# Kernel optimization log

Hardware: AMD Instinct MI355X
Metric: run time of the kernel (lower is better)

Reference implementation:

```python
import jax, jax.numpy as jnp
import numpy as np

EPS = 1e-5

def _bn(x, gamma, beta):
    # BatchNorm with track_running_stats=False: batch stats over all dims but last
    axes = tuple(range(x.ndim - 1))
    mu = jnp.mean(x, axis=axes)
    var = jnp.var(x, axis=axes)  # biased, as torch uses for normalization
    return (x - mu) * jax.lax.rsqrt(var + EPS) * gamma + beta

def setup_inputs() -> dict:
    B, N, D = 8, 200, 128
    key = jax.random.key(0)
    ks = jax.random.split(key, 14)
    s = 1.0 / np.sqrt(D)
    def w(k):
        return jax.random.uniform(k, (D, D), jnp.float32, -s, s)
    def b(k):
        return jax.random.uniform(k, (D,), jnp.float32, -s, s)
    return {
        'h': jax.random.normal(ks[0], (B, N, D), jnp.float32),
        'e': jax.random.normal(ks[1], (B, N, N, D), jnp.float32),
        'Uw': w(ks[2]), 'Ub': b(ks[3]),
        'Vw': w(ks[4]), 'Vb': b(ks[5]),
        'Aw': w(ks[6]), 'Ab': b(ks[7]),
        'Bw': w(ks[8]), 'Bb': b(ks[9]),
        'Cw': w(ks[10]), 'Cb': b(ks[11]),
        'gamma_h': jnp.ones((D,), jnp.float32), 'beta_h': jnp.zeros((D,), jnp.float32),
        'gamma_e': jnp.ones((D,), jnp.float32), 'beta_e': jnp.zeros((D,), jnp.float32),
    }

def reference(h, e, Uw, Ub, Vw, Vb, Aw, Ab, Bw, Bb, Cw, Cb,
              gamma_h, beta_h, gamma_e, beta_e):
    h_in, e_in = h, e
    Uh = h @ Uw.T + Ub                      # [B,N,D]
    Vh = h @ Vw.T + Vb                      # [B,N,D]
    Ah = h @ Aw.T + Ab
    Bh = h @ Bw.T + Bb
    Ce = e @ Cw.T + Cb                      # [B,N,N,D]
    # e_new[b,i,j,d] = Ah[b,j,d] + Bh[b,i,d] + Ce[b,i,j,d]
    e_new = Ah[:, None, :, :] + Bh[:, :, None, :] + Ce
    gates = jax.nn.sigmoid(e_new)           # [B,N,N,D]
    # sum aggregation over source nodes j with Vh broadcast over i
    agg = jnp.sum(gates * Vh[:, None, :, :], axis=2)  # [B,N,D]
    h_new = Uh + agg
    h_out = h_in + jax.nn.relu(_bn(h_new, gamma_h, beta_h))
    e_out = e_in + jax.nn.relu(_bn(e_new, gamma_e, beta_e))
    return (h_out, e_out)
```

## Files before the change

### kernel.cpp

```cpp
#include <hip/hip_runtime.h>
#include <hip/hip_bf16.h>


#define B_ 8
#define N_ 200
#define D_ 128
#define BN_ (B_*N_)
#define HN_ (BN_*D_)
#define EN_ (BN_*N_*D_)

typedef __attribute__((ext_vector_type(8))) short short8v;
typedef __attribute__((ext_vector_type(4))) short short4v;
typedef __attribute__((ext_vector_type(4))) float float4v;
typedef __attribute__((ext_vector_type(4))) unsigned int uint4v;

__device__ __forceinline__ unsigned short f2b(float f) {
  unsigned u = __float_as_uint(f);
  u += 0x7FFFu + ((u >> 16) & 1u);
  return (unsigned short)(u >> 16);
}

__global__ __launch_bounds__(256) void prelin_kernel(
    const float* __restrict__ h,
    const float* __restrict__ Uw, const float* __restrict__ Ub,
    const float* __restrict__ Vw, const float* __restrict__ Vb,
    const float* __restrict__ Aw, const float* __restrict__ Ab,
    const float* __restrict__ Bw, const float* __restrict__ Bb,
    const float* __restrict__ Cw,
    float* __restrict__ Uh, float* __restrict__ Vh,
    float* __restrict__ Ah, float* __restrict__ Bh,
    unsigned short* __restrict__ Cwbf) {
  const int tid = threadIdx.x;
  if (blockIdx.x >= 100) {
    int g = (blockIdx.x - 100) * 1024 + tid * 4;
    float4v v = *(const float4v*)(Cw + g);
    short4v s;
    s.x = (short)f2b(v.x); s.y = (short)f2b(v.y);
    s.z = (short)f2b(v.z); s.w = (short)f2b(v.w);
    *(short4v*)(Cwbf + g) = s;
    return;
  }
  const int r0 = blockIdx.x * 16;
  __shared__ float hs[16][128];
  for (int k = 0; k < 2; k++) {
    int g = k * 256 + tid;
    int row = g >> 5, col4 = g & 31;
    *(float4v*)&hs[row][col4 * 4] =
        *(const float4v*)(h + (size_t)(r0 + row) * D_ + col4 * 4);
  }
  __syncthreads();
  const int c0 = tid, c1 = tid + 256;
  const float* w0 = (c0 < 128) ? (Uw + c0 * 128) : (Vw + (c0 - 128) * 128);
  const float  b0 = (c0 < 128) ? Ub[c0] : Vb[c0 - 128];
  const float* w1 = (c1 < 384) ? (Aw + (c1 - 256) * 128) : (Bw + (c1 - 384) * 128);
  const float  b1 = (c1 < 384) ? Ab[c1 - 256] : Bb[c1 - 384];
  float acc0[16], acc1[16];
#pragma unroll
  for (int r = 0; r < 16; r++) { acc0[r] = 0.f; acc1[r] = 0.f; }
  for (int k = 0; k < 128; k += 4) {
    float4v w0v = *(const float4v*)(w0 + k);
    float4v w1v = *(const float4v*)(w1 + k);
#pragma unroll
    for (int r = 0; r < 16; r++) {
      float4v hv = *(const float4v*)&hs[r][k];
      acc0[r] = fmaf(hv.x, w0v.x, fmaf(hv.y, w0v.y, fmaf(hv.z, w0v.z, fmaf(hv.w, w0v.w, acc0[r]))));
      acc1[r] = fmaf(hv.x, w1v.x, fmaf(hv.y, w1v.y, fmaf(hv.z, w1v.z, fmaf(hv.w, w1v.w, acc1[r]))));
    }
  }
  float* dst0 = (c0 < 128) ? Uh : Vh; const int cc0 = c0 & 127;
  float* dst1 = (c1 < 384) ? Ah : Bh; const int cc1 = (c1 - 256) & 127;
#pragma unroll
  for (int r = 0; r < 16; r++) {
    dst0[(size_t)(r0 + r) * D_ + cc0] = acc0[r] + b0;
    dst1[(size_t)(r0 + r) * D_ + cc1] = acc1[r] + b1;
  }
}

template <int MODE>
__global__ __launch_bounds__(256, 2) void gemm_pass(
    const float* __restrict__ e, const unsigned short* __restrict__ Cwbf,
    const float* __restrict__ Cb, const float* __restrict__ Ah,
    const float* __restrict__ Bh, const float* __restrict__ Vh,
    float* __restrict__ agg, float* __restrict__ psum, float* __restrict__ psumsq,
    const float* __restrict__ scale_e, const float* __restrict__ shift_e,
    float* __restrict__ e_out) {
  const int tid = threadIdx.x;
  const int blk = blockIdx.x;
  const int b = blk / N_;
  const int lane = tid & 63, wz = tid >> 6;
  const int c = lane & 15, q = lane >> 4;

  __shared__ __align__(16) unsigned short Bs[128 * 136];
  __shared__ __align__(16) unsigned short As[64 * 136];
  __shared__ float base_s[128];
  __shared__ float ss_s[256];

  const uint4v* bsrc = (const uint4v*)Cwbf;
#pragma unroll
  for (int k2 = 0; k2 < 8; k2++) {
    int g = k2 * 256 + tid;
    int row = g >> 4, col = (g & 15) * 8;
    *(uint4v*)&Bs[row * 136 + col] = bsrc[g];
  }
  if (tid < 128) {
    base_s[tid] = Cb[tid] + Bh[(size_t)blk * D_ + tid];
    if (MODE == 1) { ss_s[tid] = scale_e[tid]; ss_s[128 + tid] = shift_e[tid]; }
  }

  float aggv[8], sumv[8], sqv[8];
  if (MODE == 0) {
#pragma unroll
    for (int t = 0; t < 8; t++) { aggv[t] = 0.f; sumv[t] = 0.f; sqv[t] = 0.f; }
  }

  const float* erow = e + (size_t)blk * N_ * D_;
  const float* AhB = Ah + (size_t)b * N_ * D_;
  const float* VhB = (MODE == 0) ? (Vh + (size_t)b * N_ * D_) : nullptr;

  for (int jt = 0; jt < 4; jt++) {
    const int j0 = jt * 64;
    __syncthreads();
#pragma unroll
    for (int k2 = 0; k2 < 8; k2++) {
      int g = k2 * 256 + tid;
      int row = g >> 5, col4 = g & 31;
      int j = j0 + row;
      float4v v;
      if (j < N_) v = *(const float4v*)(erow + (size_t)j * D_ + col4 * 4);
      else        v = (float4v){0.f, 0.f, 0.f, 0.f};
      short4v sv;
      sv.x = (short)f2b(v.x); sv.y = (short)f2b(v.y);
      sv.z = (short)f2b(v.z); sv.w = (short)f2b(v.w);
      *(short4v*)&As[row * 136 + col4 * 4] = sv;
    }
    __syncthreads();

    float4v acc[8];
#pragma unroll
    for (int t = 0; t < 8; t++) acc[t] = (float4v){0.f, 0.f, 0.f, 0.f};
    const unsigned short* arow = &As[(wz * 16 + c) * 136];
    const int ko = q * 8;
#pragma unroll
    for (int kk = 0; kk < 128; kk += 32) {
      short8v av = *(const short8v*)(arow + kk + ko);
#pragma unroll
      for (int t = 0; t < 8; t++) {
        short8v bv = *(const short8v*)&Bs[(t * 16 + c) * 136 + kk + ko];
        acc[t] = __builtin_amdgcn_mfma_f32_16x16x32_bf16(av, bv, acc[t], 0, 0, 0);
      }
    }

#pragma unroll
    for (int t = 0; t < 8; t++) {
      const int n = t * 16 + c;
      const float bse = base_s[n];
      float sc = 0.f, sh = 0.f;
      if (MODE == 1) { sc = ss_s[n]; sh = ss_s[128 + n]; }
#pragma unroll
      for (int r = 0; r < 4; r++) {
        const int j = j0 + wz * 16 + q * 4 + r;
        if (j < N_) {
          float x = acc[t][r] + bse + AhB[(size_t)j * D_ + n];
          if (MODE == 0) {
            float g = __builtin_amdgcn_rcpf(1.0f + __expf(-x));
            aggv[t] += g * VhB[(size_t)j * D_ + n];
            sumv[t] += x;
            sqv[t] += x * x;
          } else {
            float y = fmaxf(x * sc + sh, 0.f);
            size_t idx = (size_t)blk * N_ * D_ + (size_t)j * D_ + n;
            e_out[idx] = e[idx] + y;
          }
        }
      }
    }
  }

  if (MODE == 0) {
    __syncthreads();
    float* red = (float*)As;
#pragma unroll
    for (int t = 0; t < 8; t++) {
      float a = aggv[t], s = sumv[t], sq = sqv[t];
      a += __shfl_xor(a, 16); a += __shfl_xor(a, 32);
      s += __shfl_xor(s, 16); s += __shfl_xor(s, 32);
      sq += __shfl_xor(sq, 16); sq += __shfl_xor(sq, 32);
      if (q == 0) {
        red[(0 * 4 + wz) * 128 + t * 16 + c] = a;
        red[(1 * 4 + wz) * 128 + t * 16 + c] = s;
        red[(2 * 4 + wz) * 128 + t * 16 + c] = sq;
      }
    }
    __syncthreads();
    if (tid < 128) {
      float a = 0.f, s = 0.f, sq = 0.f;
#pragma unroll
      for (int w = 0; w < 4; w++) {
        a += red[(0 * 4 + w) * 128 + tid];
        s += red[(1 * 4 + w) * 128 + tid];
        sq += red[(2 * 4 + w) * 128 + tid];
      }
      agg[(size_t)blk * D_ + tid] = a;
      psum[(size_t)blk * D_ + tid] = s;
      psumsq[(size_t)blk * D_ + tid] = sq;
    }
  }
}

__global__ __launch_bounds__(256) void stats_kernel(
    const float* __restrict__ psum, const float* __restrict__ psumsq,
    const float* __restrict__ Uh, const float* __restrict__ agg,
    const float* __restrict__ gamma_h, const float* __restrict__ beta_h,
    const float* __restrict__ gamma_e, const float* __restrict__ beta_e,
    float* __restrict__ scale_e, float* __restrict__ shift_e,
    float* __restrict__ scale_h, float* __restrict__ shift_h) {
  const int n = blockIdx.x, t = threadIdx.x;
  float s = 0.f, sq = 0.f, hs = 0.f, hsq = 0.f;
  for (int k = t; k < BN_; k += 256) {
    s += psum[(size_t)k * D_ + n];
    sq += psumsq[(size_t)k * D_ + n];
    float hv = Uh[(size_t)k * D_ + n] + agg[(size_t)k * D_ + n];
    hs += hv; hsq += hv * hv;
  }
  __shared__ float r4[4][256];
  r4[0][t] = s; r4[1][t] = sq; r4[2][t] = hs; r4[3][t] = hsq;
  __syncthreads();
  for (int off = 128; off > 0; off >>= 1) {
    if (t < off) {
      r4[0][t] += r4[0][t + off]; r4[1][t] += r4[1][t + off];
      r4[2][t] += r4[2][t + off]; r4[3][t] += r4[3][t + off];
    }
    __syncthreads();
  }
  if (t == 0) {
    const float Me = (float)(B_ * N_ * N_);
    float mean = r4[0][0] / Me;
    float var = r4[1][0] / Me - mean * mean;
    float sce = gamma_e[n] * rsqrtf(var + 1e-5f);
    scale_e[n] = sce; shift_e[n] = beta_e[n] - mean * sce;
    const float Mh = (float)BN_;
    float mh = r4[2][0] / Mh;
    float vh = r4[3][0] / Mh - mh * mh;
    float sch = gamma_h[n] * rsqrtf(vh + 1e-5f);
    scale_h[n] = sch; shift_h[n] = beta_h[n] - mh * sch;
  }
}

__global__ __launch_bounds__(256) void hpath_kernel(
    const float* __restrict__ h, const float* __restrict__ Uh,
    const float* __restrict__ agg, const float* __restrict__ scale_h,
    const float* __restrict__ shift_h, float* __restrict__ h_out) {
  const int idx = blockIdx.x * 256 + threadIdx.x;
  float4v u = ((const float4v*)Uh)[idx];
  float4v a = ((const float4v*)agg)[idx];
  float4v hv = ((const float4v*)h)[idx];
  float4v sc = ((const float4v*)scale_h)[idx & 31];
  float4v sh = ((const float4v*)shift_h)[idx & 31];
  float4v o;
#pragma unroll
  for (int l = 0; l < 4; l++) {
    float y = fmaxf((u[l] + a[l]) * sc[l] + sh[l], 0.f);
    o[l] = hv[l] + y;
  }
  ((float4v*)h_out)[idx] = o;
}

extern "C" void kernel_launch(void* const* d_in, const int* in_sizes, int n_in,
                              void* d_out, int out_size, void* d_ws, size_t ws_size,
                              hipStream_t stream) {
  const float* h  = (const float*)d_in[0];
  const float* e  = (const float*)d_in[1];
  const float* Uw = (const float*)d_in[2];  const float* Ub = (const float*)d_in[3];
  const float* Vw = (const float*)d_in[4];  const float* Vb = (const float*)d_in[5];
  const float* Aw = (const float*)d_in[6];  const float* Ab = (const float*)d_in[7];
  const float* Bw = (const float*)d_in[8];  const float* Bb = (const float*)d_in[9];
  const float* Cw = (const float*)d_in[10]; const float* Cb = (const float*)d_in[11];
  const float* gamma_h = (const float*)d_in[12]; const float* beta_h = (const float*)d_in[13];
  const float* gamma_e = (const float*)d_in[14]; const float* beta_e = (const float*)d_in[15];

  float* ws = (float*)d_ws;
  float* Uh = ws + 0;
  float* Vh = ws + (size_t)HN_;
  float* Ah = ws + (size_t)HN_ * 2;
  float* Bh = ws + (size_t)HN_ * 3;
  float* agg = ws + (size_t)HN_ * 4;
  float* psum = ws + (size_t)HN_ * 5;
  float* psumsq = ws + (size_t)HN_ * 6;
  float* scale_e = ws + (size_t)HN_ * 7;
  float* shift_e = scale_e + 128;
  float* scale_h = scale_e + 256;
  float* shift_h = scale_e + 384;
  unsigned short* Cwbf = (unsigned short*)(scale_e + 512);

  float* h_out = (float*)d_out;
  float* e_out = (float*)d_out + HN_;

  prelin_kernel<<<116, 256, 0, stream>>>(h, Uw, Ub, Vw, Vb, Aw, Ab, Bw, Bb, Cw,
                                         Uh, Vh, Ah, Bh, Cwbf);
  gemm_pass<0><<<BN_, 256, 0, stream>>>(e, Cwbf, Cb, Ah, Bh, Vh,
                                        agg, psum, psumsq,
                                        nullptr, nullptr, nullptr);
  stats_kernel<<<128, 256, 0, stream>>>(psum, psumsq, Uh, agg,
                                        gamma_h, beta_h, gamma_e, beta_e,
                                        scale_e, shift_e, scale_h, shift_h);
  hpath_kernel<<<200, 256, 0, stream>>>(h, Uh, agg, scale_h, shift_h, h_out);
  gemm_pass<1><<<BN_, 256, 0, stream>>>(e, Cwbf, Cb, Ah, Bh, nullptr,
                                        nullptr, nullptr, nullptr,
                                        scale_e, shift_e, e_out);
}
```

Before: 571.1 us.

## Load e tiles straight into MFMA registers, vectorize e_out epilogue, split stats reduction

The GEMM pass now loads each wave's e rows directly from global memory into registers in MFMA operand layout, converting them to bf16 in place. This removes the LDS staging buffer and its per-tile barriers, and the next tile is prefetched into registers during compute. In mode 1 the MFMA operands are swapped so each lane owns four contiguous output columns, which lets the e_out read-modify-write use float4 accesses. The stats kernel is split into a coalesced 100-block partial reduction and a single-block finalize, replacing the strided column-wise reads. The trade-off is more register pressure from the prefetched tiles, at occupancy bounded by launch_bounds(256,2).

```diff
diff --git a/kernel.cpp b/kernel.cpp
--- a/kernel.cpp
+++ b/kernel.cpp
@@ -7,7 +7,6 @@
 #define D_ 128
 #define BN_ (B_*N_)
 #define HN_ (BN_*D_)
-#define EN_ (BN_*N_*D_)
 
 typedef __attribute__((ext_vector_type(8))) short short8v;
 typedef __attribute__((ext_vector_type(4))) short short4v;
@@ -91,7 +90,6 @@
   const int c = lane & 15, q = lane >> 4;
 
   __shared__ __align__(16) unsigned short Bs[128 * 136];
-  __shared__ __align__(16) unsigned short As[64 * 136];
   __shared__ float base_s[128];
   __shared__ float ss_s[256];
 
@@ -106,144 +104,197 @@
     base_s[tid] = Cb[tid] + Bh[(size_t)blk * D_ + tid];
     if (MODE == 1) { ss_s[tid] = scale_e[tid]; ss_s[128 + tid] = shift_e[tid]; }
   }
-
-  float aggv[8], sumv[8], sqv[8];
-  if (MODE == 0) {
-#pragma unroll
-    for (int t = 0; t < 8; t++) { aggv[t] = 0.f; sumv[t] = 0.f; sqv[t] = 0.f; }
-  }
+  __syncthreads();
 
   const float* erow = e + (size_t)blk * N_ * D_;
   const float* AhB = Ah + (size_t)b * N_ * D_;
   const float* VhB = (MODE == 0) ? (Vh + (size_t)b * N_ * D_) : nullptr;
 
+  float aggv[8], sumv[8], sqv[8];
+  if (MODE == 0) {
+#pragma unroll
+    for (int t = 0; t < 8; t++) { aggv[t] = 0.f; sumv[t] = 0.f; sqv[t] = 0.f; }
+  }
+
+  float4v ef[8];
+  {
+    const int j = wz * 16 + c;
+    const float* p = erow + (size_t)j * D_ + q * 8;
+    const bool ok = (j < N_);
+#pragma unroll
+    for (int l = 0; l < 4; l++) {
+      ef[2 * l]     = ok ? *(const float4v*)(p + l * 32)     : (float4v){0.f,0.f,0.f,0.f};
+      ef[2 * l + 1] = ok ? *(const float4v*)(p + l * 32 + 4) : (float4v){0.f,0.f,0.f,0.f};
+    }
+  }
+
+#pragma unroll
   for (int jt = 0; jt < 4; jt++) {
     const int j0 = jt * 64;
-    __syncthreads();
-#pragma unroll
-    for (int k2 = 0; k2 < 8; k2++) {
-      int g = k2 * 256 + tid;
-      int row = g >> 5, col4 = g & 31;
-      int j = j0 + row;
-      float4v v;
-      if (j < N_) v = *(const float4v*)(erow + (size_t)j * D_ + col4 * 4);
-      else        v = (float4v){0.f, 0.f, 0.f, 0.f};
-      short4v sv;
-      sv.x = (short)f2b(v.x); sv.y = (short)f2b(v.y);
-      sv.z = (short)f2b(v.z); sv.w = (short)f2b(v.w);
-      *(short4v*)&As[row * 136 + col4 * 4] = sv;
-    }
-    __syncthreads();
+    short8v av[4];
+#pragma unroll
+    for (int l = 0; l < 4; l++) {
+      float4v v0 = ef[2 * l], v1 = ef[2 * l + 1];
+      short8v s;
+      s[0] = (short)f2b(v0.x); s[1] = (short)f2b(v0.y);
+      s[2] = (short)f2b(v0.z); s[3] = (short)f2b(v0.w);
+      s[4] = (short)f2b(v1.x); s[5] = (short)f2b(v1.y);
+      s[6] = (short)f2b(v1.z); s[7] = (short)f2b(v1.w);
+      av[l] = s;
+    }
+    if (jt < 3) {
+      const int j = (jt + 1) * 64 + wz * 16 + c;
+      const float* p = erow + (size_t)j * D_ + q * 8;
+      const bool ok = (j < N_);
+#pragma unroll
+      for (int l = 0; l < 4; l++) {
+        ef[2 * l]     = ok ? *(const float4v*)(p + l * 32)     : (float4v){0.f,0.f,0.f,0.f};
+        ef[2 * l + 1] = ok ? *(const float4v*)(p + l * 32 + 4) : (float4v){0.f,0.f,0.f,0.f};
+      }
+    }
 
     float4v acc[8];
 #pragma unroll
     for (int t = 0; t < 8; t++) acc[t] = (float4v){0.f, 0.f, 0.f, 0.f};
-    const unsigned short* arow = &As[(wz * 16 + c) * 136];
-    const int ko = q * 8;
-#pragma unroll
-    for (int kk = 0; kk < 128; kk += 32) {
-      short8v av = *(const short8v*)(arow + kk + ko);
+#pragma unroll
+    for (int t = 0; t < 8; t++) {
+      const unsigned short* brow = &Bs[(t * 16 + c) * 136 + q * 8];
+#pragma unroll
+      for (int l = 0; l < 4; l++) {
+        short8v cw = *(const short8v*)(brow + l * 32);
+        if (MODE == 0)
+          acc[t] = __builtin_amdgcn_mfma_f32_16x16x32_bf16(av[l], cw, acc[t], 0, 0, 0);
+        else
+          acc[t] = __builtin_amdgcn_mfma_f32_16x16x32_bf16(cw, av[l], acc[t], 0, 0, 0);
+      }
+    }
+
+    if (MODE == 0) {
 #pragma unroll
       for (int t = 0; t < 8; t++) {
-        short8v bv = *(const short8v*)&Bs[(t * 16 + c) * 136 + kk + ko];
-        acc[t] = __builtin_amdgcn_mfma_f32_16x16x32_bf16(av, bv, acc[t], 0, 0, 0);
-      }
-    }
-
-#pragma unroll
-    for (int t = 0; t < 8; t++) {
-      const int n = t * 16 + c;
-      const float bse = base_s[n];
-      float sc = 0.f, sh = 0.f;
-      if (MODE == 1) { sc = ss_s[n]; sh = ss_s[128 + n]; }
-#pragma unroll
-      for (int r = 0; r < 4; r++) {
-        const int j = j0 + wz * 16 + q * 4 + r;
-        if (j < N_) {
-          float x = acc[t][r] + bse + AhB[(size_t)j * D_ + n];
-          if (MODE == 0) {
+        const int n = t * 16 + c;
+        const float bse = base_s[n];
+#pragma unroll
+        for (int r = 0; r < 4; r++) {
+          const int j = j0 + wz * 16 + q * 4 + r;
+          if (j < N_) {
+            float x = acc[t][r] + bse + AhB[(size_t)j * D_ + n];
             float g = __builtin_amdgcn_rcpf(1.0f + __expf(-x));
             aggv[t] += g * VhB[(size_t)j * D_ + n];
             sumv[t] += x;
             sqv[t] += x * x;
-          } else {
-            float y = fmaxf(x * sc + sh, 0.f);
-            size_t idx = (size_t)blk * N_ * D_ + (size_t)j * D_ + n;
-            e_out[idx] = e[idx] + y;
           }
         }
       }
+    } else {
+      const int j = j0 + wz * 16 + c;
+      if (j < N_) {
+        const size_t rowoff = (size_t)blk * N_ * D_ + (size_t)j * D_;
+#pragma unroll
+        for (int t = 0; t < 8; t++) {
+          const int n4 = t * 16 + q * 4;
+          float4v ah = *(const float4v*)(AhB + (size_t)j * D_ + n4);
+          float4v bs4 = *(const float4v*)&base_s[n4];
+          float4v sc4 = *(const float4v*)&ss_s[n4];
+          float4v sh4 = *(const float4v*)&ss_s[128 + n4];
+          float4v ein = *(const float4v*)(e + rowoff + n4);
+          float4v o;
+#pragma unroll
+          for (int r = 0; r < 4; r++) {
+            float x = acc[t][r] + bs4[r] + ah[r];
+            float y = fmaxf(x * sc4[r] + sh4[r], 0.f);
+            o[r] = ein[r] + y;
+          }
+          *(float4v*)(e_out + rowoff + n4) = o;
+        }
+      }
     }
   }
 
   if (MODE == 0) {
     __syncthreads();
-    float* red = (float*)As;
+    float* red = (float*)Bs;
 #pragma unroll
     for (int t = 0; t < 8; t++) {
-      float a = aggv[t], s = sumv[t], sq = sqv[t];
+      float a = aggv[t], s = sumv[t], sq2 = sqv[t];
       a += __shfl_xor(a, 16); a += __shfl_xor(a, 32);
       s += __shfl_xor(s, 16); s += __shfl_xor(s, 32);
-      sq += __shfl_xor(sq, 16); sq += __shfl_xor(sq, 32);
+      sq2 += __shfl_xor(sq2, 16); sq2 += __shfl_xor(sq2, 32);
       if (q == 0) {
         red[(0 * 4 + wz) * 128 + t * 16 + c] = a;
         red[(1 * 4 + wz) * 128 + t * 16 + c] = s;
-        red[(2 * 4 + wz) * 128 + t * 16 + c] = sq;
+        red[(2 * 4 + wz) * 128 + t * 16 + c] = sq2;
       }
     }
     __syncthreads();
     if (tid < 128) {
-      float a = 0.f, s = 0.f, sq = 0.f;
+      float a = 0.f, s = 0.f, sq2 = 0.f;
 #pragma unroll
       for (int w = 0; w < 4; w++) {
         a += red[(0 * 4 + w) * 128 + tid];
         s += red[(1 * 4 + w) * 128 + tid];
-        sq += red[(2 * 4 + w) * 128 + tid];
+        sq2 += red[(2 * 4 + w) * 128 + tid];
       }
       agg[(size_t)blk * D_ + tid] = a;
       psum[(size_t)blk * D_ + tid] = s;
-      psumsq[(size_t)blk * D_ + tid] = sq;
-    }
-  }
-}
-
-__global__ __launch_bounds__(256) void stats_kernel(
+      psumsq[(size_t)blk * D_ + tid] = sq2;
+    }
+  }
+}
+
+__global__ __launch_bounds__(256) void stats_part(
     const float* __restrict__ psum, const float* __restrict__ psumsq,
     const float* __restrict__ Uh, const float* __restrict__ agg,
+    float* __restrict__ partial) {
+  const int t = threadIdx.x, blk = blockIdx.x;
+  const int cg = t & 31, rs = t >> 5;
+  float4v ps = {0,0,0,0}, pq = {0,0,0,0}, hs = {0,0,0,0}, hq = {0,0,0,0};
+#pragma unroll
+  for (int p = 0; p < 2; p++) {
+    const int row = blk * 16 + p * 8 + rs;
+    const size_t off = (size_t)row * D_ + cg * 4;
+    float4v a = *(const float4v*)(psum + off);
+    float4v bq = *(const float4v*)(psumsq + off);
+    float4v u = *(const float4v*)(Uh + off);
+    float4v g = *(const float4v*)(agg + off);
+    ps += a; pq += bq;
+    float4v hv = u + g;
+    hs += hv; hq += hv * hv;
+  }
+  __shared__ float4v red[4][8][32];
+  red[0][rs][cg] = ps; red[1][rs][cg] = pq; red[2][rs][cg] = hs; red[3][rs][cg] = hq;
+  __syncthreads();
+  if (t < 128) {
+    const int s = t >> 5, g = t & 31;
+    float4v acc = red[s][0][g];
+#pragma unroll
+    for (int r = 1; r < 8; r++) acc += red[s][r][g];
+    *(float4v*)(partial + (size_t)blk * 512 + s * 128 + g * 4) = acc;
+  }
+}
+
+__global__ __launch_bounds__(128) void stats_final(
+    const float* __restrict__ partial,
     const float* __restrict__ gamma_h, const float* __restrict__ beta_h,
     const float* __restrict__ gamma_e, const float* __restrict__ beta_e,
     float* __restrict__ scale_e, float* __restrict__ shift_e,
     float* __restrict__ scale_h, float* __restrict__ shift_h) {
-  const int n = blockIdx.x, t = threadIdx.x;
-  float s = 0.f, sq = 0.f, hs = 0.f, hsq = 0.f;
-  for (int k = t; k < BN_; k += 256) {
-    s += psum[(size_t)k * D_ + n];
-    sq += psumsq[(size_t)k * D_ + n];
-    float hv = Uh[(size_t)k * D_ + n] + agg[(size_t)k * D_ + n];
-    hs += hv; hsq += hv * hv;
-  }
-  __shared__ float r4[4][256];
-  r4[0][t] = s; r4[1][t] = sq; r4[2][t] = hs; r4[3][t] = hsq;
-  __syncthreads();
-  for (int off = 128; off > 0; off >>= 1) {
-    if (t < off) {
-      r4[0][t] += r4[0][t + off]; r4[1][t] += r4[1][t + off];
-      r4[2][t] += r4[2][t + off]; r4[3][t] += r4[3][t + off];
-    }
-    __syncthreads();
-  }
-  if (t == 0) {
-    const float Me = (float)(B_ * N_ * N_);
-    float mean = r4[0][0] / Me;
-    float var = r4[1][0] / Me - mean * mean;
-    float sce = gamma_e[n] * rsqrtf(var + 1e-5f);
-    scale_e[n] = sce; shift_e[n] = beta_e[n] - mean * sce;
-    const float Mh = (float)BN_;
-    float mh = r4[2][0] / Mh;
-    float vh = r4[3][0] / Mh - mh * mh;
-    float sch = gamma_h[n] * rsqrtf(vh + 1e-5f);
-    scale_h[n] = sch; shift_h[n] = beta_h[n] - mh * sch;
-  }
+  const int n = threadIdx.x;
+  float s = 0.f, sq = 0.f, hs = 0.f, hq = 0.f;
+  for (int p = 0; p < 100; p++) {
+    const float* base = partial + (size_t)p * 512;
+    s += base[n]; sq += base[128 + n]; hs += base[256 + n]; hq += base[384 + n];
+  }
+  const float Me = 8.f * 200.f * 200.f;
+  float mean = s / Me;
+  float var = sq / Me - mean * mean;
+  float sce = gamma_e[n] * rsqrtf(var + 1e-5f);
+  scale_e[n] = sce; shift_e[n] = beta_e[n] - mean * sce;
+  const float Mh = (float)BN_;
+  float mh = hs / Mh;
+  float vh = hq / Mh - mh * mh;
+  float sch = gamma_h[n] * rsqrtf(vh + 1e-5f);
+  scale_h[n] = sch; shift_h[n] = beta_h[n] - mh * sch;
 }
 
 __global__ __launch_bounds__(256) void hpath_kernel(
@@ -291,6 +342,7 @@
   float* scale_h = scale_e + 256;
   float* shift_h = scale_e + 384;
   unsigned short* Cwbf = (unsigned short*)(scale_e + 512);
+  float* partial = scale_e + 512 + 8192;
 
   float* h_out = (float*)d_out;
   float* e_out = (float*)d_out + HN_;
@@ -300,9 +352,9 @@
   gemm_pass<0><<<BN_, 256, 0, stream>>>(e, Cwbf, Cb, Ah, Bh, Vh,
                                         agg, psum, psumsq,
                                         nullptr, nullptr, nullptr);
-  stats_kernel<<<128, 256, 0, stream>>>(psum, psumsq, Uh, agg,
-                                        gamma_h, beta_h, gamma_e, beta_e,
-                                        scale_e, shift_e, scale_h, shift_h);
+  stats_part<<<100, 256, 0, stream>>>(psum, psumsq, Uh, agg, partial);
+  stats_final<<<1, 128, 0, stream>>>(partial, gamma_h, beta_h, gamma_e, beta_e,
+                                     scale_e, shift_e, scale_h, shift_h);
   hpath_kernel<<<200, 256, 0, stream>>>(h, Uh, agg, scale_h, shift_h, h_out);
   gemm_pass<1><<<BN_, 256, 0, stream>>>(e, Cwbf, Cb, Ah, Bh, nullptr,
                                         nullptr, nullptr, nullptr,
```

Measured after the change: 484.7 us. 15.1% less time.
